# Performance work log

Measured on AMD Instinct MI355X. Metric: run time of the kernel, lower is better.

## Reference

```python
import jax, jax.numpy as jnp
import numpy as np

WINDOW_SIZE = 11
SIGMA = 1.5
CHANNEL = 3


def _gaussian_window(window_size, sigma, channel):
    x = np.arange(window_size, dtype=np.float32)
    g = np.exp(-((x - window_size // 2) ** 2) / (2.0 * sigma ** 2))
    g = g / g.sum()
    w2d = np.outer(g, g).astype(np.float32)  # (ws, ws)
    # depthwise kernel: (C, 1, ws, ws) in OIHW with feature_group_count=C
    return jnp.asarray(np.broadcast_to(w2d, (channel, 1, window_size, window_size)).copy())


def _dwconv(x, w, pad):
    # x: (N, C, H, W), w: (C, 1, kh, kw), depthwise 'same' conv
    return jax.lax.conv_general_dilated(
        x, w, window_strides=(1, 1), padding=[(pad, pad), (pad, pad)],
        dimension_numbers=("NCHW", "OIHW", "NCHW"),
        feature_group_count=x.shape[1])


def setup_inputs() -> dict:
    key = jax.random.key(0)
    k1, k2 = jax.random.split(key)
    img1 = jax.random.uniform(k1, (32, 3, 512, 512), dtype=jnp.float32)
    img2 = jax.random.uniform(k2, (32, 3, 512, 512), dtype=jnp.float32)
    window = _gaussian_window(WINDOW_SIZE, SIGMA, CHANNEL)
    return {"img1": img1, "img2": img2, "window": window}


def reference(img1, img2, window):
    pad = WINDOW_SIZE // 2
    mu1 = _dwconv(img1, window, pad)
    mu2 = _dwconv(img2, window, pad)
    mu1_sq = mu1 * mu1
    mu2_sq = mu2 * mu2
    mu1_mu2 = mu1 * mu2
    sigma1_sq = _dwconv(img1 * img1, window, pad) - mu1_sq
    sigma2_sq = _dwconv(img2 * img2, window, pad) - mu2_sq
    sigma12 = _dwconv(img1 * img2, window, pad) - mu1_mu2

    C1 = 0.01 ** 2
    C2 = 0.03 ** 2
    C3 = C2 / 2.0

    a1 = jnp.abs(sigma1_sq)
    a2 = jnp.abs(sigma2_sq)
    s1 = jnp.sqrt(a1)
    s2 = jnp.sqrt(a2)

    L = (2.0 * mu1_mu2 + C1) / (mu1_sq + mu2_sq + C1)
    C = (2.0 * s1 * s2 + C2) / (a1 + a2 + C2)
    S = (sigma12 + C3) / (s1 * s2 + C3)

    return (L.mean(), C.mean(), S.mean())
```

## Files before the change

kernel.cpp:

```cpp
#include <hip/hip_runtime.h>
#include <math.h>

#define IMG 512
#define PLANES 96
#define XS_W 54
#define NXS 10
#define YS_H 64
#define NYS 8
#define WPB 4
#define NSLOT 32
#define ACC_STRIDE 16
#define INV_NPIX (1.0 / 25165824.0)


__global__ void ssim_init(double* __restrict__ acc, float* __restrict__ gwp,
                          const float* __restrict__ win) {
    int i = threadIdx.x;
    if (i < NSLOT * ACC_STRIDE) acc[i] = 0.0;
    if (i < 11) gwp[i] = sqrtf(win[i * 12]);
}

template<int P>
__device__ __forceinline__ void row_step(
    int T, int y0, bool col_ok,
    const float* __restrict__ p1, const float* __restrict__ p2,
    float& x1, float& x2, const int (&si)[11], const float* __restrict__ g,
    float (&A)[5][11], bool out_ok, float& sL, float& sC, float& sS)
{
    const int t = T + P;
    const int gy_next = y0 - 4 + t;
    float nx1 = 0.f, nx2 = 0.f;
    if (col_ok && (unsigned)gy_next < IMG) {
        int off = gy_next * IMG;
        nx1 = p1[off];
        nx2 = p2[off];
    }
    float a[11], b[11];
    #pragma unroll
    for (int j = 0; j < 11; ++j) {
        if (j == 5) { a[j] = x1; b[j] = x2; }
        else {
            a[j] = __int_as_float(__builtin_amdgcn_ds_bpermute(si[j], __float_as_int(x1)));
            b[j] = __int_as_float(__builtin_amdgcn_ds_bpermute(si[j], __float_as_int(x2)));
        }
    }
    float H1 = 0.f, H2 = 0.f, H11 = 0.f, H22 = 0.f, H12 = 0.f;
    #pragma unroll
    for (int j = 0; j < 11; ++j) {
        float w = g[j];
        float t1 = w * a[j], t2 = w * b[j];
        H1 += t1; H2 += t2;
        H11 = fmaf(t1, a[j], H11);
        H22 = fmaf(t2, b[j], H22);
        H12 = fmaf(t1, b[j], H12);
    }
    #pragma unroll
    for (int j = 0; j < 11; ++j) {
        const int s = (P + j + 1) % 11;
        float w = g[10 - j];
        A[0][s] = fmaf(w, H1,  A[0][s]);
        A[1][s] = fmaf(w, H2,  A[1][s]);
        A[2][s] = fmaf(w, H11, A[2][s]);
        A[3][s] = fmaf(w, H22, A[3][s]);
        A[4][s] = fmaf(w, H12, A[4][s]);
    }
    const int es = (P + 1) % 11;
    if (t >= 10 && t <= 73) {
        float mu1 = A[0][es], mu2 = A[1][es];
        float x11 = A[2][es], x22 = A[3][es], x12 = A[4][es];
        float mu1s = mu1 * mu1, mu2s = mu2 * mu2, mu12 = mu1 * mu2;
        float v1 = x11 - mu1s, v2 = x22 - mu2s, v12 = x12 - mu12;
        float a1 = fabsf(v1), a2 = fabsf(v2);
        float q12 = sqrtf(a1 * a2);
        const float C1 = 1e-4f, C2 = 9e-4f, C3 = 4.5e-4f;
        float eL = __fdividef(2.f * mu12 + C1, mu1s + mu2s + C1);
        float eC = __fdividef(2.f * q12 + C2, a1 + a2 + C2);
        float eS = __fdividef(v12 + C3, q12 + C3);
        if (out_ok) { sL += eL; sC += eC; sS += eS; }
    }
    #pragma unroll
    for (int q = 0; q < 5; ++q) A[q][es] = 0.f;
    x1 = nx1; x2 = nx2;
}

__global__ __launch_bounds__(256, 4) void ssim_main(
    const float* __restrict__ img1, const float* __restrict__ img2,
    const float* __restrict__ gwp, double* __restrict__ acc)
{
    const int lane = threadIdx.x & 63;
    const int wid  = blockIdx.x * WPB + (threadIdx.x >> 6);
    const int plane = wid / (NXS * NYS);
    const int rem   = wid % (NXS * NYS);
    const int ys = rem / NXS, xs = rem % NXS;
    const int x0 = xs * XS_W;
    const int y0 = ys * YS_H;
    const int col = x0 - 5 + lane;
    const bool col_ok = (unsigned)col < IMG;
    const bool out_ok = (lane >= 5) && (lane <= 58) && col_ok;

    const float* g = gwp;

    int si[11];
    #pragma unroll
    for (int j = 0; j < 11; ++j) si[j] = (lane + j - 5) << 2;

    const float* p1 = img1 + (size_t)plane * (IMG * IMG) + col;
    const float* p2 = img2 + (size_t)plane * (IMG * IMG) + col;

    float x1 = 0.f, x2 = 0.f;
    {
        int gy = y0 - 5;
        if (col_ok && (unsigned)gy < IMG) { x1 = p1[gy * IMG]; x2 = p2[gy * IMG]; }
    }

    float A[5][11];
    #pragma unroll
    for (int q = 0; q < 5; ++q)
        #pragma unroll
        for (int s = 0; s < 11; ++s) A[q][s] = 0.f;

    float sL = 0.f, sC = 0.f, sS = 0.f;

    #pragma unroll 1
    for (int T = 0; T < 66; T += 11) {
        row_step<0>(T, y0, col_ok, p1, p2, x1, x2, si, g, A, out_ok, sL, sC, sS);
        row_step<1>(T, y0, col_ok, p1, p2, x1, x2, si, g, A, out_ok, sL, sC, sS);
        row_step<2>(T, y0, col_ok, p1, p2, x1, x2, si, g, A, out_ok, sL, sC, sS);
        row_step<3>(T, y0, col_ok, p1, p2, x1, x2, si, g, A, out_ok, sL, sC, sS);
        row_step<4>(T, y0, col_ok, p1, p2, x1, x2, si, g, A, out_ok, sL, sC, sS);
        row_step<5>(T, y0, col_ok, p1, p2, x1, x2, si, g, A, out_ok, sL, sC, sS);
        row_step<6>(T, y0, col_ok, p1, p2, x1, x2, si, g, A, out_ok, sL, sC, sS);
        row_step<7>(T, y0, col_ok, p1, p2, x1, x2, si, g, A, out_ok, sL, sC, sS);
        row_step<8>(T, y0, col_ok, p1, p2, x1, x2, si, g, A, out_ok, sL, sC, sS);
        row_step<9>(T, y0, col_ok, p1, p2, x1, x2, si, g, A, out_ok, sL, sC, sS);
        row_step<10>(T, y0, col_ok, p1, p2, x1, x2, si, g, A, out_ok, sL, sC, sS);
    }
    row_step<0>(66, y0, col_ok, p1, p2, x1, x2, si, g, A, out_ok, sL, sC, sS);
    row_step<1>(66, y0, col_ok, p1, p2, x1, x2, si, g, A, out_ok, sL, sC, sS);
    row_step<2>(66, y0, col_ok, p1, p2, x1, x2, si, g, A, out_ok, sL, sC, sS);
    row_step<3>(66, y0, col_ok, p1, p2, x1, x2, si, g, A, out_ok, sL, sC, sS);
    row_step<4>(66, y0, col_ok, p1, p2, x1, x2, si, g, A, out_ok, sL, sC, sS);
    row_step<5>(66, y0, col_ok, p1, p2, x1, x2, si, g, A, out_ok, sL, sC, sS);
    row_step<6>(66, y0, col_ok, p1, p2, x1, x2, si, g, A, out_ok, sL, sC, sS);
    row_step<7>(66, y0, col_ok, p1, p2, x1, x2, si, g, A, out_ok, sL, sC, sS);

    #pragma unroll
    for (int off = 32; off > 0; off >>= 1) {
        sL += __shfl_down(sL, off, 64);
        sC += __shfl_down(sC, off, 64);
        sS += __shfl_down(sS, off, 64);
    }
    if (lane == 0) {
        double* slot = acc + (size_t)(wid & (NSLOT - 1)) * ACC_STRIDE;
        atomicAdd(slot + 0, (double)sL);
        atomicAdd(slot + 1, (double)sC);
        atomicAdd(slot + 2, (double)sS);
    }
}

__global__ void ssim_fin(const double* __restrict__ acc, float* __restrict__ out) {
    int i = threadIdx.x;
    if (i < 3) {
        double s = 0.0;
        for (int k = 0; k < NSLOT; ++k) s += acc[k * ACC_STRIDE + i];
        out[i] = (float)(s * INV_NPIX);
    }
}

extern "C" void kernel_launch(void* const* d_in, const int* in_sizes, int n_in,
                              void* d_out, int out_size, void* d_ws, size_t ws_size,
                              hipStream_t stream) {
    const float* img1 = (const float*)d_in[0];
    const float* img2 = (const float*)d_in[1];
    const float* win  = (const float*)d_in[2];
    float* out = (float*)d_out;
    double* acc = (double*)d_ws;
    float* gwp = (float*)((char*)d_ws + NSLOT * ACC_STRIDE * sizeof(double));

    ssim_init<<<1, 512, 0, stream>>>(acc, gwp, win);
    ssim_main<<<(PLANES * NXS * NYS) / WPB, 64 * WPB, 0, stream>>>(img1, img2, gwp, acc);
    ssim_fin<<<1, 64, 0, stream>>>(acc, out);
}
```

Before: 332.3 us.

## Process row pairs with packed FP32 FMA for separable SSIM convolution

Restructures the vertical sliding-window accumulation to handle two image rows per step, using packed two-wide float FMAs for the horizontal and vertical passes. The ring of accumulators shrinks from 11 scalar slots to 6 paired slots, and the vertical taps are rearranged into paired weight vectors. The aim is to halve the VALU instruction count on packed-math hardware. Register pressure rises, so launch bounds drop to 3 waves per SIMD. The ds_bpermute count per row is unchanged.

```diff
diff --git a/kernel.cpp b/kernel.cpp
--- a/kernel.cpp
+++ b/kernel.cpp
@@ -12,6 +12,8 @@
 #define ACC_STRIDE 16
 #define INV_NPIX (1.0 / 25165824.0)
 
+typedef float f32x2 __attribute__((ext_vector_type(2)));
+
 
 __global__ void ssim_init(double* __restrict__ acc, float* __restrict__ gwp,
                           const float* __restrict__ win) {
@@ -20,70 +22,99 @@
     if (i < 11) gwp[i] = sqrtf(win[i * 12]);
 }
 
+static __device__ __forceinline__ f32x2 pk_fma(f32x2 a, f32x2 b, f32x2 c) {
+    return __builtin_elementwise_fma(a, b, c);
+}
+static __device__ __forceinline__ f32x2 splat_lo(f32x2 v) { f32x2 r; r.x = v.x; r.y = v.x; return r; }
+static __device__ __forceinline__ f32x2 splat_hi(f32x2 v) { f32x2 r; r.x = v.y; r.y = v.y; return r; }
+
+static __device__ __forceinline__ f32x2 bperm_pair(int idx, f32x2 v) {
+    f32x2 r;
+    r.x = __int_as_float(__builtin_amdgcn_ds_bpermute(idx, __float_as_int(v.x)));
+    r.y = __int_as_float(__builtin_amdgcn_ds_bpermute(idx, __float_as_int(v.y)));
+    return r;
+}
+
+static __device__ __forceinline__ void emit_row(
+    float mu1s, float mu2s, float mu12, float x11, float x22, float x12,
+    bool ok, float& sL, float& sC, float& sS)
+{
+    float v1 = x11 - mu1s, v2 = x22 - mu2s, v12 = x12 - mu12;
+    float a1 = fabsf(v1), a2 = fabsf(v2);
+    float q12 = sqrtf(a1 * a2);
+    const float C1 = 1e-4f, C2 = 9e-4f, C3 = 4.5e-4f;
+    float eL = __fdividef(2.f * mu12 + C1, mu1s + mu2s + C1);
+    float eC = __fdividef(2.f * q12 + C2, a1 + a2 + C2);
+    float eS = __fdividef(v12 + C3, q12 + C3);
+    if (ok) { sL += eL; sC += eC; sS += eS; }
+}
+
 template<int P>
-__device__ __forceinline__ void row_step(
-    int T, int y0, bool col_ok,
+__device__ __forceinline__ void pair_step(
+    int u, int y0, bool col_ok,
     const float* __restrict__ p1, const float* __restrict__ p2,
-    float& x1, float& x2, const int (&si)[11], const float* __restrict__ g,
-    float (&A)[5][11], bool out_ok, float& sL, float& sC, float& sS)
+    f32x2& x1p, f32x2& x2p, const int (&si)[11],
+    const f32x2 (&g2h)[6], const f32x2 (&wA)[6], const f32x2 (&wB)[6],
+    f32x2 (&A)[5][6], bool out_ok, float& sL, float& sC, float& sS)
 {
-    const int t = T + P;
-    const int gy_next = y0 - 4 + t;
-    float nx1 = 0.f, nx2 = 0.f;
-    if (col_ok && (unsigned)gy_next < IMG) {
-        int off = gy_next * IMG;
-        nx1 = p1[off];
-        nx2 = p2[off];
-    }
-    float a[11], b[11];
+    const int gya = y0 - 3 + 2 * u;
+    const int gyb = gya + 1;
+    f32x2 nx1 = {0.f, 0.f}, nx2 = {0.f, 0.f};
+    if (col_ok && (unsigned)gya < IMG) { int o = gya * IMG; nx1.x = p1[o]; nx2.x = p2[o]; }
+    if (col_ok && (unsigned)gyb < IMG) { int o = gyb * IMG; nx1.y = p1[o]; nx2.y = p2[o]; }
+
+    f32x2 H1 = {0.f,0.f}, H2 = {0.f,0.f}, H11 = {0.f,0.f}, H22 = {0.f,0.f}, H12 = {0.f,0.f};
     #pragma unroll
     for (int j = 0; j < 11; ++j) {
-        if (j == 5) { a[j] = x1; b[j] = x2; }
-        else {
-            a[j] = __int_as_float(__builtin_amdgcn_ds_bpermute(si[j], __float_as_int(x1)));
-            b[j] = __int_as_float(__builtin_amdgcn_ds_bpermute(si[j], __float_as_int(x2)));
-        }
-    }
-    float H1 = 0.f, H2 = 0.f, H11 = 0.f, H22 = 0.f, H12 = 0.f;
-    #pragma unroll
-    for (int j = 0; j < 11; ++j) {
-        float w = g[j];
-        float t1 = w * a[j], t2 = w * b[j];
-        H1 += t1; H2 += t2;
-        H11 = fmaf(t1, a[j], H11);
-        H22 = fmaf(t2, b[j], H22);
-        H12 = fmaf(t1, b[j], H12);
-    }
-    #pragma unroll
-    for (int j = 0; j < 11; ++j) {
-        const int s = (P + j + 1) % 11;
-        float w = g[10 - j];
-        A[0][s] = fmaf(w, H1,  A[0][s]);
-        A[1][s] = fmaf(w, H2,  A[1][s]);
-        A[2][s] = fmaf(w, H11, A[2][s]);
-        A[3][s] = fmaf(w, H22, A[3][s]);
-        A[4][s] = fmaf(w, H12, A[4][s]);
-    }
-    const int es = (P + 1) % 11;
-    if (t >= 10 && t <= 73) {
-        float mu1 = A[0][es], mu2 = A[1][es];
-        float x11 = A[2][es], x22 = A[3][es], x12 = A[4][es];
-        float mu1s = mu1 * mu1, mu2s = mu2 * mu2, mu12 = mu1 * mu2;
-        float v1 = x11 - mu1s, v2 = x22 - mu2s, v12 = x12 - mu12;
-        float a1 = fabsf(v1), a2 = fabsf(v2);
-        float q12 = sqrtf(a1 * a2);
-        const float C1 = 1e-4f, C2 = 9e-4f, C3 = 4.5e-4f;
-        float eL = __fdividef(2.f * mu12 + C1, mu1s + mu2s + C1);
-        float eC = __fdividef(2.f * q12 + C2, a1 + a2 + C2);
-        float eS = __fdividef(v12 + C3, q12 + C3);
-        if (out_ok) { sL += eL; sC += eC; sS += eS; }
-    }
-    #pragma unroll
-    for (int q = 0; q < 5; ++q) A[q][es] = 0.f;
-    x1 = nx1; x2 = nx2;
-}
-
-__global__ __launch_bounds__(256, 4) void ssim_main(
+        const int hj = (j <= 5) ? j : 10 - j;
+        f32x2 aj, bj;
+        if (j == 5) { aj = x1p; bj = x2p; }
+        else        { aj = bperm_pair(si[j], x1p); bj = bperm_pair(si[j], x2p); }
+        f32x2 t1 = g2h[hj] * aj;
+        f32x2 t2 = g2h[hj] * bj;
+        H1  = H1 + t1;
+        H2  = H2 + t2;
+        H11 = pk_fma(t1, aj, H11);
+        H22 = pk_fma(t2, bj, H22);
+        H12 = pk_fma(t1, bj, H12);
+    }
+
+    const f32x2 H1l = splat_lo(H1),  H1h = splat_hi(H1);
+    const f32x2 H2l = splat_lo(H2),  H2h = splat_hi(H2);
+    const f32x2 Hal = splat_lo(H11), Hah = splat_hi(H11);
+    const f32x2 Hbl = splat_lo(H22), Hbh = splat_hi(H22);
+    const f32x2 Hcl = splat_lo(H12), Hch = splat_hi(H12);
+    #pragma unroll
+    for (int e = 0; e < 6; ++e) {
+        const int s = (P - e + 6) % 6;
+        A[0][s] = pk_fma(H1l, wA[e], A[0][s]);
+        A[0][s] = pk_fma(H1h, wB[e], A[0][s]);
+        A[1][s] = pk_fma(H2l, wA[e], A[1][s]);
+        A[1][s] = pk_fma(H2h, wB[e], A[1][s]);
+        A[2][s] = pk_fma(Hal, wA[e], A[2][s]);
+        A[2][s] = pk_fma(Hah, wB[e], A[2][s]);
+        A[3][s] = pk_fma(Hbl, wA[e], A[3][s]);
+        A[3][s] = pk_fma(Hbh, wB[e], A[3][s]);
+        A[4][s] = pk_fma(Hcl, wA[e], A[4][s]);
+        A[4][s] = pk_fma(Hch, wB[e], A[4][s]);
+    }
+
+    const int es = (P + 1) % 6;
+    if (u >= 5) {
+        f32x2 mu1 = A[0][es], mu2 = A[1][es];
+        f32x2 x11 = A[2][es], x22 = A[3][es], x12 = A[4][es];
+        f32x2 mu1s = mu1 * mu1;
+        f32x2 mu2s = mu2 * mu2;
+        f32x2 mu12 = mu1 * mu2;
+        emit_row(mu1s.x, mu2s.x, mu12.x, x11.x, x22.x, x12.x, out_ok, sL, sC, sS);
+        emit_row(mu1s.y, mu2s.y, mu12.y, x11.y, x22.y, x12.y, out_ok, sL, sC, sS);
+    }
+    #pragma unroll
+    for (int q = 0; q < 5; ++q) { A[q][es].x = 0.f; A[q][es].y = 0.f; }
+    x1p = nx1; x2p = nx2;
+}
+
+__global__ __launch_bounds__(256, 3) void ssim_main(
     const float* __restrict__ img1, const float* __restrict__ img2,
     const float* __restrict__ gwp, double* __restrict__ acc)
 {
@@ -98,51 +129,53 @@
     const bool col_ok = (unsigned)col < IMG;
     const bool out_ok = (lane >= 5) && (lane <= 58) && col_ok;
 
-    const float* g = gwp;
-
     int si[11];
     #pragma unroll
     for (int j = 0; j < 11; ++j) si[j] = (lane + j - 5) << 2;
+
+    float gj[11];
+    #pragma unroll
+    for (int j = 0; j < 11; ++j) gj[j] = gwp[j];
+    f32x2 g2h[6];
+    #pragma unroll
+    for (int j = 0; j < 6; ++j) { g2h[j].x = gj[j]; g2h[j].y = gj[j]; }
+    f32x2 wA[6], wB[6];
+    #pragma unroll
+    for (int e = 0; e < 6; ++e) {
+        wA[e].x = gj[2*e];
+        wA[e].y = (e == 0) ? 0.f : gj[2*e - 1];
+        wB[e].x = (e == 5) ? 0.f : gj[2*e + 1];
+        wB[e].y = gj[2*e];
+    }
 
     const float* p1 = img1 + (size_t)plane * (IMG * IMG) + col;
     const float* p2 = img2 + (size_t)plane * (IMG * IMG) + col;
 
-    float x1 = 0.f, x2 = 0.f;
+    f32x2 x1p = {0.f, 0.f}, x2p = {0.f, 0.f};
     {
-        int gy = y0 - 5;
-        if (col_ok && (unsigned)gy < IMG) { x1 = p1[gy * IMG]; x2 = p2[gy * IMG]; }
-    }
-
-    float A[5][11];
+        int ga = y0 - 5, gb = y0 - 4;
+        if (col_ok && (unsigned)ga < IMG) { int o = ga * IMG; x1p.x = p1[o]; x2p.x = p2[o]; }
+        if (col_ok && (unsigned)gb < IMG) { int o = gb * IMG; x1p.y = p1[o]; x2p.y = p2[o]; }
+    }
+
+    f32x2 A[5][6];
     #pragma unroll
     for (int q = 0; q < 5; ++q)
         #pragma unroll
-        for (int s = 0; s < 11; ++s) A[q][s] = 0.f;
+        for (int s = 0; s < 6; ++s) { A[q][s].x = 0.f; A[q][s].y = 0.f; }
 
     float sL = 0.f, sC = 0.f, sS = 0.f;
 
     #pragma unroll 1
-    for (int T = 0; T < 66; T += 11) {
-        row_step<0>(T, y0, col_ok, p1, p2, x1, x2, si, g, A, out_ok, sL, sC, sS);
-        row_step<1>(T, y0, col_ok, p1, p2, x1, x2, si, g, A, out_ok, sL, sC, sS);
-        row_step<2>(T, y0, col_ok, p1, p2, x1, x2, si, g, A, out_ok, sL, sC, sS);
-        row_step<3>(T, y0, col_ok, p1, p2, x1, x2, si, g, A, out_ok, sL, sC, sS);
-        row_step<4>(T, y0, col_ok, p1, p2, x1, x2, si, g, A, out_ok, sL, sC, sS);
-        row_step<5>(T, y0, col_ok, p1, p2, x1, x2, si, g, A, out_ok, sL, sC, sS);
-        row_step<6>(T, y0, col_ok, p1, p2, x1, x2, si, g, A, out_ok, sL, sC, sS);
-        row_step<7>(T, y0, col_ok, p1, p2, x1, x2, si, g, A, out_ok, sL, sC, sS);
-        row_step<8>(T, y0, col_ok, p1, p2, x1, x2, si, g, A, out_ok, sL, sC, sS);
-        row_step<9>(T, y0, col_ok, p1, p2, x1, x2, si, g, A, out_ok, sL, sC, sS);
-        row_step<10>(T, y0, col_ok, p1, p2, x1, x2, si, g, A, out_ok, sL, sC, sS);
-    }
-    row_step<0>(66, y0, col_ok, p1, p2, x1, x2, si, g, A, out_ok, sL, sC, sS);
-    row_step<1>(66, y0, col_ok, p1, p2, x1, x2, si, g, A, out_ok, sL, sC, sS);
-    row_step<2>(66, y0, col_ok, p1, p2, x1, x2, si, g, A, out_ok, sL, sC, sS);
-    row_step<3>(66, y0, col_ok, p1, p2, x1, x2, si, g, A, out_ok, sL, sC, sS);
-    row_step<4>(66, y0, col_ok, p1, p2, x1, x2, si, g, A, out_ok, sL, sC, sS);
-    row_step<5>(66, y0, col_ok, p1, p2, x1, x2, si, g, A, out_ok, sL, sC, sS);
-    row_step<6>(66, y0, col_ok, p1, p2, x1, x2, si, g, A, out_ok, sL, sC, sS);
-    row_step<7>(66, y0, col_ok, p1, p2, x1, x2, si, g, A, out_ok, sL, sC, sS);
+    for (int U = 0; U < 36; U += 6) {
+        pair_step<0>(U+0, y0, col_ok, p1, p2, x1p, x2p, si, g2h, wA, wB, A, out_ok, sL, sC, sS);
+        pair_step<1>(U+1, y0, col_ok, p1, p2, x1p, x2p, si, g2h, wA, wB, A, out_ok, sL, sC, sS);
+        pair_step<2>(U+2, y0, col_ok, p1, p2, x1p, x2p, si, g2h, wA, wB, A, out_ok, sL, sC, sS);
+        pair_step<3>(U+3, y0, col_ok, p1, p2, x1p, x2p, si, g2h, wA, wB, A, out_ok, sL, sC, sS);
+        pair_step<4>(U+4, y0, col_ok, p1, p2, x1p, x2p, si, g2h, wA, wB, A, out_ok, sL, sC, sS);
+        pair_step<5>(U+5, y0, col_ok, p1, p2, x1p, x2p, si, g2h, wA, wB, A, out_ok, sL, sC, sS);
+    }
+    pair_step<0>(36, y0, col_ok, p1, p2, x1p, x2p, si, g2h, wA, wB, A, out_ok, sL, sC, sS);
 
     #pragma unroll
     for (int off = 32; off > 0; off >>= 1) {
```

Result: slower. 341.9 us (+2.9%).

## Drop init kernel, compute weights in-kernel, replace atomics with per-block partials

Applied to the files above, without the earlier changes.

Removes the separate init kernel by computing the separable Gaussian weights inside the main kernel, keeping them in registers and making them wave-uniform with readfirstlane. Double-precision atomics are replaced by a per-block shared-memory reduction that writes float4 partials, and a larger final kernel tree-reduces those partials. The ring accumulator no longer needs explicit zeroing, because the last tap now overwrites the slot, and the first horizontal tap becomes a plain multiply. This saves one launch, the atomic traffic and some ALU work, at the cost of float-precision per-block partial sums.

```diff
diff --git a/kernel.cpp b/kernel.cpp
--- a/kernel.cpp
+++ b/kernel.cpp
@@ -8,23 +8,19 @@
 #define YS_H 64
 #define NYS 8
 #define WPB 4
-#define NSLOT 32
-#define ACC_STRIDE 16
+#define NBLK ((PLANES * NXS * NYS) / WPB)
 #define INV_NPIX (1.0 / 25165824.0)
 
 
-__global__ void ssim_init(double* __restrict__ acc, float* __restrict__ gwp,
-                          const float* __restrict__ win) {
-    int i = threadIdx.x;
-    if (i < NSLOT * ACC_STRIDE) acc[i] = 0.0;
-    if (i < 11) gwp[i] = sqrtf(win[i * 12]);
+static __device__ __forceinline__ float rfl(float x) {
+    return __int_as_float(__builtin_amdgcn_readfirstlane(__float_as_int(x)));
 }
 
 template<int P>
 __device__ __forceinline__ void row_step(
     int T, int y0, bool col_ok,
     const float* __restrict__ p1, const float* __restrict__ p2,
-    float& x1, float& x2, const int (&si)[11], const float* __restrict__ g,
+    float& x1, float& x2, const int (&si)[11], const float (&g)[11],
     float (&A)[5][11], bool out_ok, float& sL, float& sC, float& sS)
 {
     const int t = T + P;
@@ -44,11 +40,13 @@
             b[j] = __int_as_float(__builtin_amdgcn_ds_bpermute(si[j], __float_as_int(x2)));
         }
     }
-    float H1 = 0.f, H2 = 0.f, H11 = 0.f, H22 = 0.f, H12 = 0.f;
-    #pragma unroll
-    for (int j = 0; j < 11; ++j) {
+    float t1 = g[0] * a[0], t2 = g[0] * b[0];
+    float H1 = t1, H2 = t2;
+    float H11 = t1 * a[0], H22 = t2 * b[0], H12 = t1 * b[0];
+    #pragma unroll
+    for (int j = 1; j < 11; ++j) {
         float w = g[j];
-        float t1 = w * a[j], t2 = w * b[j];
+        t1 = w * a[j]; t2 = w * b[j];
         H1 += t1; H2 += t2;
         H11 = fmaf(t1, a[j], H11);
         H22 = fmaf(t2, b[j], H22);
@@ -58,11 +56,19 @@
     for (int j = 0; j < 11; ++j) {
         const int s = (P + j + 1) % 11;
         float w = g[10 - j];
-        A[0][s] = fmaf(w, H1,  A[0][s]);
-        A[1][s] = fmaf(w, H2,  A[1][s]);
-        A[2][s] = fmaf(w, H11, A[2][s]);
-        A[3][s] = fmaf(w, H22, A[3][s]);
-        A[4][s] = fmaf(w, H12, A[4][s]);
+        if (j == 10) {
+            A[0][s] = w * H1;
+            A[1][s] = w * H2;
+            A[2][s] = w * H11;
+            A[3][s] = w * H22;
+            A[4][s] = w * H12;
+        } else {
+            A[0][s] = fmaf(w, H1,  A[0][s]);
+            A[1][s] = fmaf(w, H2,  A[1][s]);
+            A[2][s] = fmaf(w, H11, A[2][s]);
+            A[3][s] = fmaf(w, H22, A[3][s]);
+            A[4][s] = fmaf(w, H12, A[4][s]);
+        }
     }
     const int es = (P + 1) % 11;
     if (t >= 10 && t <= 73) {
@@ -78,17 +84,16 @@
         float eS = __fdividef(v12 + C3, q12 + C3);
         if (out_ok) { sL += eL; sC += eC; sS += eS; }
     }
-    #pragma unroll
-    for (int q = 0; q < 5; ++q) A[q][es] = 0.f;
     x1 = nx1; x2 = nx2;
 }
 
 __global__ __launch_bounds__(256, 4) void ssim_main(
     const float* __restrict__ img1, const float* __restrict__ img2,
-    const float* __restrict__ gwp, double* __restrict__ acc)
+    const float* __restrict__ win, float4* __restrict__ part)
 {
     const int lane = threadIdx.x & 63;
-    const int wid  = blockIdx.x * WPB + (threadIdx.x >> 6);
+    const int widx = threadIdx.x >> 6;
+    const int wid  = blockIdx.x * WPB + widx;
     const int plane = wid / (NXS * NYS);
     const int rem   = wid % (NXS * NYS);
     const int ys = rem / NXS, xs = rem % NXS;
@@ -98,7 +103,9 @@
     const bool col_ok = (unsigned)col < IMG;
     const bool out_ok = (lane >= 5) && (lane <= 58) && col_ok;
 
-    const float* g = gwp;
+    float g[11];
+    #pragma unroll
+    for (int j = 0; j < 11; ++j) g[j] = rfl(sqrtf(win[j * 12]));
 
     int si[11];
     #pragma unroll
@@ -150,21 +157,36 @@
         sC += __shfl_down(sC, off, 64);
         sS += __shfl_down(sS, off, 64);
     }
-    if (lane == 0) {
-        double* slot = acc + (size_t)(wid & (NSLOT - 1)) * ACC_STRIDE;
-        atomicAdd(slot + 0, (double)sL);
-        atomicAdd(slot + 1, (double)sC);
-        atomicAdd(slot + 2, (double)sS);
-    }
-}
-
-__global__ void ssim_fin(const double* __restrict__ acc, float* __restrict__ out) {
-    int i = threadIdx.x;
-    if (i < 3) {
-        double s = 0.0;
-        for (int k = 0; k < NSLOT; ++k) s += acc[k * ACC_STRIDE + i];
-        out[i] = (float)(s * INV_NPIX);
-    }
+    __shared__ float red[WPB][4];
+    if (lane == 0) { red[widx][0] = sL; red[widx][1] = sC; red[widx][2] = sS; }
+    __syncthreads();
+    if (threadIdx.x == 0) {
+        float L = 0.f, C = 0.f, S = 0.f;
+        #pragma unroll
+        for (int w = 0; w < WPB; ++w) { L += red[w][0]; C += red[w][1]; S += red[w][2]; }
+        part[blockIdx.x] = make_float4(L, C, S, 0.f);
+    }
+}
+
+__global__ void ssim_fin(const float4* __restrict__ part, float* __restrict__ out) {
+    const int t = threadIdx.x;
+    double L = 0.0, C = 0.0, S = 0.0;
+    for (int i = t; i < NBLK; i += 256) {
+        float4 p = part[i];
+        L += (double)p.x; C += (double)p.y; S += (double)p.z;
+    }
+    __shared__ double red[256][3];
+    red[t][0] = L; red[t][1] = C; red[t][2] = S;
+    __syncthreads();
+    for (int s = 128; s > 0; s >>= 1) {
+        if (t < s) {
+            red[t][0] += red[t + s][0];
+            red[t][1] += red[t + s][1];
+            red[t][2] += red[t + s][2];
+        }
+        __syncthreads();
+    }
+    if (t < 3) out[t] = (float)(red[0][t] * INV_NPIX);
 }
 
 extern "C" void kernel_launch(void* const* d_in, const int* in_sizes, int n_in,
@@ -174,10 +196,8 @@
     const float* img2 = (const float*)d_in[1];
     const float* win  = (const float*)d_in[2];
     float* out = (float*)d_out;
-    double* acc = (double*)d_ws;
-    float* gwp = (float*)((char*)d_ws + NSLOT * ACC_STRIDE * sizeof(double));
-
-    ssim_init<<<1, 512, 0, stream>>>(acc, gwp, win);
-    ssim_main<<<(PLANES * NXS * NYS) / WPB, 64 * WPB, 0, stream>>>(img1, img2, gwp, acc);
-    ssim_fin<<<1, 64, 0, stream>>>(acc, out);
-}
+    float4* part = (float4*)d_ws;
+
+    ssim_main<<<NBLK, 64 * WPB, 0, stream>>>(img1, img2, win, part);
+    ssim_fin<<<1, 256, 0, stream>>>(part, out);
+}
```

New measurement: 333.2 us. Within noise of the previous version (+0.3%).
